# Performance work log

Measured on AMD Instinct MI355X. Metric: run time of the kernel, lower is better.

The kernel has to match this reference:

```python
import jax, jax.numpy as jnp
import numpy as np

B, T, C, H = 4, 1024, 1024, 16
D = C // H  # head dim = 64
EPS = 1e-5


def _layernorm(x, g, b):
    m = jnp.mean(x, axis=-1, keepdims=True)
    v = jnp.var(x, axis=-1, keepdims=True)
    return (x - m) / jnp.sqrt(v + EPS) * g + b


def setup_inputs() -> dict:
    key = jax.random.key(0)
    ks = jax.random.split(key, 8)
    s = 0.02  # GPT-style init scale
    w = lambda k, shp: (jax.random.normal(k, shp, jnp.float32) * s)
    return {
        "x": jax.random.normal(ks[0], (B, T, C), jnp.float32),
        "ln1_g": jnp.ones((C,), jnp.float32), "ln1_b": jnp.zeros((C,), jnp.float32),
        "wq": w(ks[1], (C, C)), "bq": jnp.zeros((C,), jnp.float32),
        "wk": w(ks[2], (C, C)), "bk": jnp.zeros((C,), jnp.float32),
        "wv": w(ks[3], (C, C)), "bv": jnp.zeros((C,), jnp.float32),
        "wo": w(ks[4], (C, C)), "bo": jnp.zeros((C,), jnp.float32),
        "ln2_g": jnp.ones((C,), jnp.float32), "ln2_b": jnp.zeros((C,), jnp.float32),
        "w1": w(ks[5], (C, 4 * C)), "b1": jnp.zeros((4 * C,), jnp.float32),
        "w2": w(ks[6], (4 * C, C)), "b2": jnp.zeros((C,), jnp.float32),
    }


def reference(x, ln1_g, ln1_b, wq, bq, wk, bk, wv, bv, wo, bo,
              ln2_g, ln2_b, w1, b1, w2, b2):
    # --- causal self-attention branch: x = x + attn(ln1(x)) ---
    h = _layernorm(x, ln1_g, ln1_b)
    q = (h @ wq + bq).reshape(B, T, H, D)
    k = (h @ wk + bk).reshape(B, T, H, D)
    v = (h @ wv + bv).reshape(B, T, H, D)
    att = jnp.einsum('bqhd,bkhd->bhqk', q, k) * (1.0 / np.sqrt(D).astype(np.float32))
    causal = jnp.tril(jnp.ones((T, T), bool))
    att = jnp.where(causal, att, -jnp.inf)
    att = jax.nn.softmax(att, axis=-1)  # dropout p=0 -> identity
    y = jnp.einsum('bhqk,bkhd->bqhd', att, v).reshape(B, T, C)
    x = x + (y @ wo + bo)
    # --- MLP branch: x = x + mlp(ln2(x)) ---
    h2 = _layernorm(x, ln2_g, ln2_b)
    m = jax.nn.gelu(h2 @ w1 + b1, approximate=False)  # torch nn.GELU default = exact erf
    x = x + (m @ w2 + b2)
    return x
```

## Files before the change

### kernel.cpp

```cpp
#include <hip/hip_runtime.h>
#include <hip/hip_bf16.h>
#include <math.h>

#define B_ 4
#define T_ 1024
#define C_ 1024
#define H_ 16
#define D_ 64
#define M_ (B_*T_)

typedef __bf16 bf16;
typedef __bf16 bf16x8 __attribute__((ext_vector_type(8)));
typedef float  f32x4  __attribute__((ext_vector_type(4)));

#define MFMA16(a, b, c) __builtin_amdgcn_mfma_f32_16x16x32_bf16((a), (b), (c), 0, 0, 0)

__device__ __forceinline__ void gload16(const void* g, void* l) {
  __builtin_amdgcn_global_load_lds((const __attribute__((address_space(1))) void*)g,
                                   (__attribute__((address_space(3))) void*)l,
                                   16, 0, 0);
}

__global__ __launch_bounds__(256) void wconvT(const float* __restrict__ W,
                                              bf16* __restrict__ WT, int K, int N) {
  __shared__ float tile[32][33];
  int n0 = blockIdx.x * 32, k0 = blockIdx.y * 32;
  int tx = threadIdx.x & 31, ty = threadIdx.x >> 5;
#pragma unroll
  for (int i = ty; i < 32; i += 8)
    tile[i][tx] = W[(size_t)(k0 + i) * N + n0 + tx];
  __syncthreads();
#pragma unroll
  for (int i = ty; i < 32; i += 8)
    WT[(size_t)(n0 + i) * K + k0 + tx] = (bf16)tile[tx][i];
}

__global__ __launch_bounds__(256) void bcat(const float* __restrict__ a,
                                            const float* __restrict__ b,
                                            const float* __restrict__ c,
                                            float* __restrict__ o) {
  int i = blockIdx.x * 256 + threadIdx.x;
  o[i] = (i < 1024) ? a[i] : ((i < 2048) ? b[i - 1024] : c[i - 2048]);
}

__global__ __launch_bounds__(256) void ln_k(const float* __restrict__ x,
                                            const float* __restrict__ g,
                                            const float* __restrict__ b,
                                            bf16* __restrict__ out) {
  int row = blockIdx.x;
  int t = threadIdx.x;
  float4 xv = ((const float4*)(x + (size_t)row * C_))[t];
  float s  = xv.x + xv.y + xv.z + xv.w;
  float ss = xv.x*xv.x + xv.y*xv.y + xv.z*xv.z + xv.w*xv.w;
#pragma unroll
  for (int m = 32; m; m >>= 1) { s += __shfl_xor(s, m); ss += __shfl_xor(ss, m); }
  __shared__ float red[8];
  int wid = t >> 6;
  if ((t & 63) == 0) { red[wid] = s; red[4 + wid] = ss; }
  __syncthreads();
  s  = red[0] + red[1] + red[2] + red[3];
  ss = red[4] + red[5] + red[6] + red[7];
  float mean = s * (1.0f / C_);
  float var  = ss * (1.0f / C_) - mean * mean;
  float inv  = rsqrtf(var + 1e-5f);
  float4 gv = ((const float4*)g)[t];
  float4 bv = ((const float4*)b)[t];
  bf16* o = out + (size_t)row * C_ + t * 4;
  o[0] = (bf16)((xv.x - mean) * inv * gv.x + bv.x);
  o[1] = (bf16)((xv.y - mean) * inv * gv.y + bv.y);
  o[2] = (bf16)((xv.z - mean) * inv * gv.z + bv.z);
  o[3] = (bf16)((xv.w - mean) * inv * gv.w + bv.w);
}

template <int BM, int BN, int WM, int WN, int EPI>
__global__ __launch_bounds__(WM*WN*64, 4)
void gemms(const bf16* __restrict__ A, const bf16* __restrict__ BT,
           const float* __restrict__ bias, const float* __restrict__ res,
           void* __restrict__ outp, int N, int K, int gx) {
  constexpr int NT = WM * WN * 64;
  constexpr int FM = BM / WM / 16, FN = BN / WN / 16;
  constexpr int RA = BM / 32, RB = BN / 32;
  __shared__ __align__(16) bf16 smem[(BM + BN) * 64];
  bf16* sA = smem;
  bf16* sB = smem + BM * 64;
  const int tid = threadIdx.x, lane = tid & 63, wid = tid >> 6;
  const int wr = wid / WN, wc = wid % WN;

  int bid = blockIdx.x;
  const int nwg = gridDim.x;
  if (!(nwg & 7)) bid = (bid & 7) * (nwg >> 3) + (bid >> 3);
  const int bx = bid % gx, by = bid / gx;
  const size_t am0 = (size_t)bx * BM, bn0 = (size_t)by * BN;

  f32x4 acc[FM][FN];
  const f32x4 fz = {0.f, 0.f, 0.f, 0.f};
#pragma unroll
  for (int m = 0; m < FM; ++m)
#pragma unroll
    for (int n = 0; n < FN; ++n) acc[m][n] = fz;

  const int srow = tid >> 3;
  const int sg = (tid & 7) ^ (srow & 7);
  const bf16* ag = A  + (am0 + srow) * (size_t)K + sg * 8;
  const bf16* bg = BT + (bn0 + srow) * (size_t)K + sg * 8;

  const int arow = lane & 15;
  const int g0 = (((lane >> 4))     ^ (lane & 7)) * 8;
  const int g1 = (((lane >> 4) + 4) ^ (lane & 7)) * 8;
  const int nt = K >> 6;

#pragma unroll
  for (int r = 0; r < RA; ++r)
    gload16(ag + (size_t)(r * 32) * K, sA + r * 2048 + tid * 8);
#pragma unroll
  for (int r = 0; r < RB; ++r)
    gload16(bg + (size_t)(r * 32) * K, sB + r * 2048 + tid * 8);

  for (int t = 0; t < nt; ++t) {
    __syncthreads();

    const bf16* pa = sA + (wr * (BM / WM) + arow) * 64;
    const bf16* pb = sB + (wc * (BN / WN) + arow) * 64;
    bf16x8 a[FM], b[FN];
#pragma unroll
    for (int m = 0; m < FM; ++m) a[m] = *(const bf16x8*)(pa + m * 16 * 64 + g0);
#pragma unroll
    for (int n = 0; n < FN; ++n) b[n] = *(const bf16x8*)(pb + n * 16 * 64 + g0);
#pragma unroll
    for (int m = 0; m < FM; ++m)
#pragma unroll
      for (int n = 0; n < FN; ++n)
        acc[m][n] = MFMA16(a[m], b[n], acc[m][n]);
    bf16x8 a1[FM], b1[FN];
#pragma unroll
    for (int m = 0; m < FM; ++m) a1[m] = *(const bf16x8*)(pa + m * 16 * 64 + g1);
#pragma unroll
    for (int n = 0; n < FN; ++n) b1[n] = *(const bf16x8*)(pb + n * 16 * 64 + g1);

    __syncthreads();

    if (t + 1 < nt) {
#pragma unroll
      for (int r = 0; r < RA; ++r)
        gload16(ag + (size_t)(t + 1) * 64 + (size_t)(r * 32) * K,
                sA + r * 2048 + tid * 8);
#pragma unroll
      for (int r = 0; r < RB; ++r)
        gload16(bg + (size_t)(t + 1) * 64 + (size_t)(r * 32) * K,
                sB + r * 2048 + tid * 8);
    }
#pragma unroll
    for (int m = 0; m < FM; ++m)
#pragma unroll
      for (int n = 0; n < FN; ++n)
        acc[m][n] = MFMA16(a1[m], b1[n], acc[m][n]);
  }

  if constexpr (EPI != 2) {
#pragma unroll
    for (int m = 0; m < FM; ++m) {
      const int row0 = wr * (BM / WM) + m * 16 + (lane >> 4) * 4;
#pragma unroll
      for (int n = 0; n < FN; ++n) {
        const int col = wc * (BN / WN) + n * 16 + (lane & 15);
        const float bv = bias[bn0 + col];
#pragma unroll
        for (int j = 0; j < 4; ++j) {
          float v = acc[m][n][j] + bv;
          if constexpr (EPI == 1) v = 0.5f * v * (1.0f + erff(v * 0.70710678118f));
          const int rr = row0 + j;
          smem[rr * BN + (((col >> 3) ^ (rr & 7)) << 3) + (col & 7)] = (bf16)v;
        }
      }
    }
    __syncthreads();
    constexpr int GR = BN / 8;
    constexpr int SI = BM * BN / (NT * 8);
#pragma unroll
    for (int i = 0; i < SI; ++i) {
      const int idx = i * NT + tid;
      const int row = idx / GR, g = idx % GR;
      *(bf16x8*)((bf16*)outp + (am0 + row) * N + bn0 + g * 8) =
          *(const bf16x8*)(smem + row * BN + ((g ^ (row & 7)) << 3));
    }
  } else {
    constexpr int PR = BM / WM;
    float* sf = (float*)smem;
#pragma unroll
    for (int h = 0; h < WM; ++h) {
      __syncthreads();
      if (wr == h) {
#pragma unroll
        for (int m = 0; m < FM; ++m) {
          const int lr0 = m * 16 + (lane >> 4) * 4;
#pragma unroll
          for (int n = 0; n < FN; ++n) {
            const int col = wc * (BN / WN) + n * 16 + (lane & 15);
            const float bv = bias[bn0 + col];
#pragma unroll
            for (int j = 0; j < 4; ++j)
              sf[(lr0 + j) * BN + col] = acc[m][n][j] + bv;
          }
        }
      }
      __syncthreads();
      constexpr int SI = PR * BN / (NT * 4);
#pragma unroll
      for (int i = 0; i < SI; ++i) {
        const int flat = (i * NT + tid) * 4;
        const int row = flat / BN, c = flat % BN;
        const size_t gi = (am0 + h * PR + row) * N + bn0 + c;
        float4 rv = *(const float4*)(res + gi);
        float4 sv = *(const float4*)(sf + row * BN + c);
        rv.x += sv.x; rv.y += sv.y; rv.z += sv.z; rv.w += sv.w;
        *(float4*)((float*)outp + gi) = rv;
      }
    }
  }
}

__global__ __launch_bounds__(256) void attn_k(const bf16* __restrict__ Q,
                                              const bf16* __restrict__ Kb,
                                              const bf16* __restrict__ Vb,
                                              bf16* __restrict__ Y, int ld) {
  int bh = blockIdx.x;
  int b = bh >> 4, h = bh & 15;
  int qt = (int)gridDim.y - 1 - (int)blockIdx.y;
  int q0 = qt * 64;
  int tid = threadIdx.x, wid = tid >> 6, lane = tid & 63;

  __shared__ __align__(16) bf16 sK[64 * 64];
  __shared__ __align__(16) bf16 sVT[64 * 64];
  __shared__ __align__(16) bf16 sP[4][16 * 64];

  const size_t rowQ = (size_t)(b * T_ + q0 + wid * 16 + (lane & 15)) * ld + h * 64 + (lane >> 4) * 8;
  bf16x8 qf0 = *(const bf16x8*)(Q + rowQ);
  bf16x8 qf1 = *(const bf16x8*)(Q + rowQ + 32);

  float m_run[4] = {-1e30f, -1e30f, -1e30f, -1e30f};
  float l_run[4] = {0.f, 0.f, 0.f, 0.f};
  const f32x4 fz = {0.f, 0.f, 0.f, 0.f};
  f32x4 o[4];
#pragma unroll
  for (int i = 0; i < 4; ++i) o[i] = fz;

  const int kgr = (lane & 7) ^ (lane >> 3);
  const bf16* kg = Kb + (size_t)(b * T_ + wid * 16 + (lane >> 3)) * ld + h * 64 + kgr * 8;
  bf16* lk = sK + (wid * 16) * 64;

  const int g0 = (((lane >> 4))     ^ (lane & 7)) * 8;
  const int g1 = (((lane >> 4) + 4) ^ (lane & 7)) * 8;

  for (int kt = 0; kt <= qt; ++kt) {
    int k0 = kt * 64;
#pragma unroll
    for (int i = 0; i < 2; ++i)
      gload16(kg + ((size_t)(k0 + i * 8)) * ld, lk + i * 8 * 64);
#pragma unroll
    for (int c = 0; c < 2; ++c) {
      const int r = lane, sl = wid + 4 * c;
      bf16x8 vv = *(const bf16x8*)(Vb + (size_t)(b * T_ + k0 + r) * ld + h * 64 + sl * 8);
#pragma unroll
      for (int j = 0; j < 8; ++j)
        sVT[(sl * 8 + j) * 64 + ((((r >> 3) ^ j) << 3) | (r & 7))] = vv[j];
    }
    __syncthreads();

    f32x4 s[4];
#pragma unroll
    for (int ni = 0; ni < 4; ++ni) {
      const bf16* kr = sK + (ni * 16 + (lane & 15)) * 64;
      bf16x8 kf0 = *(const bf16x8*)(kr + g0);
      bf16x8 kf1 = *(const bf16x8*)(kr + g1);
      f32x4 t = fz;
      t = MFMA16(qf0, kf0, t);
      t = MFMA16(qf1, kf1, t);
      s[ni] = t;
    }

    int rbase = q0 + wid * 16 + (lane >> 4) * 4;
    int cbase = k0 + (lane & 15);
    float tm[4] = {-1e30f, -1e30f, -1e30f, -1e30f};
#pragma unroll
    for (int ni = 0; ni < 4; ++ni)
#pragma unroll
      for (int j = 0; j < 4; ++j) {
        float v = s[ni][j] * 0.125f;
        if (cbase + ni * 16 > rbase + j) v = -1e30f;
        s[ni][j] = v;
        tm[j] = fmaxf(tm[j], v);
      }
#pragma unroll
    for (int j = 0; j < 4; ++j)
#pragma unroll
      for (int mk = 1; mk < 16; mk <<= 1)
        tm[j] = fmaxf(tm[j], __shfl_xor(tm[j], mk));

    float fac[4], rs[4] = {0.f, 0.f, 0.f, 0.f};
#pragma unroll
    for (int j = 0; j < 4; ++j) {
      float mn = fmaxf(m_run[j], tm[j]);
      fac[j] = __expf(m_run[j] - mn);
      m_run[j] = mn;
    }
#pragma unroll
    for (int ni = 0; ni < 4; ++ni)
#pragma unroll
      for (int j = 0; j < 4; ++j) {
        float p = __expf(s[ni][j] - m_run[j]);
        rs[j] += p;
        const int crow = (lane >> 4) * 4 + j;
        const int cg = (ni * 2 + ((lane & 15) >> 3)) ^ (crow & 7);
        sP[wid][crow * 64 + (cg << 3) + (lane & 7)] = (bf16)p;
      }
#pragma unroll
    for (int j = 0; j < 4; ++j) {
#pragma unroll
      for (int mk = 1; mk < 16; mk <<= 1)
        rs[j] += __shfl_xor(rs[j], mk);
      l_run[j] = l_run[j] * fac[j] + rs[j];
    }
#pragma unroll
    for (int df = 0; df < 4; ++df)
#pragma unroll
      for (int j = 0; j < 4; ++j)
        o[df][j] *= fac[j];

#pragma unroll
    for (int kk = 0; kk < 2; ++kk) {
      const int gk = kk ? g1 : g0;
      bf16x8 pf = *(const bf16x8*)(sP[wid] + (lane & 15) * 64 + gk);
#pragma unroll
      for (int df = 0; df < 4; ++df) {
        bf16x8 vf = *(const bf16x8*)(sVT + (df * 16 + (lane & 15)) * 64 + gk);
        o[df] = MFMA16(pf, vf, o[df]);
      }
    }
    __syncthreads();
  }

#pragma unroll
  for (int df = 0; df < 4; ++df)
#pragma unroll
    for (int j = 0; j < 4; ++j) {
      int row = q0 + wid * 16 + (lane >> 4) * 4 + j;
      int d = df * 16 + (lane & 15);
      Y[(size_t)(b * T_ + row) * C_ + h * 64 + d] = (bf16)(o[df][j] / l_run[j]);
    }
}

extern "C" void kernel_launch(void* const* d_in, const int* in_sizes, int n_in,
                              void* d_out, int out_size, void* d_ws, size_t ws_size,
                              hipStream_t stream) {
  (void)in_sizes; (void)n_in; (void)out_size; (void)ws_size;
  const float* x    = (const float*)d_in[0];
  const float* ln1g = (const float*)d_in[1];
  const float* ln1b = (const float*)d_in[2];
  const float* wq   = (const float*)d_in[3];
  const float* bq   = (const float*)d_in[4];
  const float* wk   = (const float*)d_in[5];
  const float* bk   = (const float*)d_in[6];
  const float* wv   = (const float*)d_in[7];
  const float* bv   = (const float*)d_in[8];
  const float* wo   = (const float*)d_in[9];
  const float* bo   = (const float*)d_in[10];
  const float* ln2g = (const float*)d_in[11];
  const float* ln2b = (const float*)d_in[12];
  const float* w1   = (const float*)d_in[13];
  const float* b1   = (const float*)d_in[14];
  const float* w2   = (const float*)d_in[15];
  const float* b2   = (const float*)d_in[16];

  char* ws = (char*)d_ws;
  const size_t MB = 1024 * 1024;
  bf16* WqkvT = (bf16*)(ws +  0 * MB);
  bf16* WoT   = (bf16*)(ws +  6 * MB);
  bf16* W1T   = (bf16*)(ws +  8 * MB);
  bf16* W2T   = (bf16*)(ws + 16 * MB);
  bf16* hbuf  = (bf16*)(ws + 24 * MB);
  bf16* qkv   = (bf16*)(ws + 32 * MB);
  bf16* yb    = (bf16*)(ws + 56 * MB);
  bf16* mb    = (bf16*)(ws + 32 * MB);
  float* x1   = (float*)(ws + 64 * MB);
  float* bqkv = (float*)d_out;

  dim3 blk(256);
  wconvT<<<dim3(32, 32),  blk, 0, stream>>>(wq, WqkvT,                 1024, 1024);
  wconvT<<<dim3(32, 32),  blk, 0, stream>>>(wk, WqkvT + 1024 * 1024,   1024, 1024);
  wconvT<<<dim3(32, 32),  blk, 0, stream>>>(wv, WqkvT + 2048 * 1024,   1024, 1024);
  wconvT<<<dim3(32, 32),  blk, 0, stream>>>(wo, WoT, 1024, 1024);
  wconvT<<<dim3(128, 32), blk, 0, stream>>>(w1, W1T, 1024, 4096);
  wconvT<<<dim3(32, 128), blk, 0, stream>>>(w2, W2T, 4096, 1024);
  bcat<<<12, blk, 0, stream>>>(bq, bk, bv, bqkv);

  ln_k<<<M_, blk, 0, stream>>>(x, ln1g, ln1b, hbuf);
  gemms<128,128,2,2,0><<<768,  blk, 0, stream>>>(hbuf, WqkvT, bqkv, nullptr, qkv, 3072, 1024, 32);
  attn_k<<<dim3(64, 16), blk, 0, stream>>>(qkv, qkv + 1024, qkv + 2048, yb, 3072);
  gemms<64,128,2,2,2><<<512,   blk, 0, stream>>>(yb, WoT, bo, x, x1, 1024, 1024, 64);
  ln_k<<<M_, blk, 0, stream>>>(x1, ln2g, ln2b, hbuf);
  gemms<128,128,2,2,1><<<1024, blk, 0, stream>>>(hbuf, W1T, b1, nullptr, mb, 4096, 1024, 32);
  gemms<64,128,2,2,2><<<512,   blk, 0, stream>>>(mb, W2T, b2, x1, (float*)d_out, 1024, 4096, 64);
}
```

Measured before the change: 232.7 us.

## Double-buffer K/V tiles in attention and merge weight conversions into one launch

```diff
diff --git a/kernel.cpp b/kernel.cpp
--- a/kernel.cpp
+++ b/kernel.cpp
@@ -21,11 +21,30 @@
                                    16, 0, 0);
 }
 
-__global__ __launch_bounds__(256) void wconvT(const float* __restrict__ W,
-                                              bf16* __restrict__ WT, int K, int N) {
+__global__ __launch_bounds__(256) void wprep(const float* __restrict__ wq,
+                                             const float* __restrict__ wk,
+                                             const float* __restrict__ wv,
+                                             const float* __restrict__ wo,
+                                             const float* __restrict__ w1,
+                                             const float* __restrict__ w2,
+                                             bf16* __restrict__ WqkvT,
+                                             bf16* __restrict__ WoT,
+                                             bf16* __restrict__ W1T,
+                                             bf16* __restrict__ W2T) {
   __shared__ float tile[32][33];
-  int n0 = blockIdx.x * 32, k0 = blockIdx.y * 32;
-  int tx = threadIdx.x & 31, ty = threadIdx.x >> 5;
+  const int b = blockIdx.x;
+  const float* W; bf16* WT; int K, N, n0, k0;
+  if (b < 3072)      { const int w = b >> 10, t = b & 1023;
+                       W = (w == 0) ? wq : ((w == 1) ? wk : wv);
+                       WT = WqkvT + (size_t)w * 1024 * 1024;
+                       K = 1024; N = 1024; n0 = (t & 31) * 32; k0 = (t >> 5) * 32; }
+  else if (b < 4096) { const int t = b - 3072; W = wo; WT = WoT;
+                       K = 1024; N = 1024; n0 = (t & 31) * 32; k0 = (t >> 5) * 32; }
+  else if (b < 8192) { const int t = b - 4096; W = w1; WT = W1T;
+                       K = 1024; N = 4096; n0 = (t & 127) * 32; k0 = (t >> 7) * 32; }
+  else               { const int t = b - 8192; W = w2; WT = W2T;
+                       K = 4096; N = 1024; n0 = (t & 31) * 32; k0 = (t >> 5) * 32; }
+  const int tx = threadIdx.x & 31, ty = threadIdx.x >> 5;
 #pragma unroll
   for (int i = ty; i < 32; i += 8)
     tile[i][tx] = W[(size_t)(k0 + i) * N + n0 + tx];
@@ -229,8 +248,8 @@
   int q0 = qt * 64;
   int tid = threadIdx.x, wid = tid >> 6, lane = tid & 63;
 
-  __shared__ __align__(16) bf16 sK[64 * 64];
-  __shared__ __align__(16) bf16 sVT[64 * 64];
+  __shared__ __align__(16) bf16 sK[2][64 * 64];
+  __shared__ __align__(16) bf16 sVT[2][64 * 64];
   __shared__ __align__(16) bf16 sP[4][16 * 64];
 
   const size_t rowQ = (size_t)(b * T_ + q0 + wid * 16 + (lane & 15)) * ld + h * 64 + (lane >> 4) * 8;
@@ -246,30 +265,44 @@
 
   const int kgr = (lane & 7) ^ (lane >> 3);
   const bf16* kg = Kb + (size_t)(b * T_ + wid * 16 + (lane >> 3)) * ld + h * 64 + kgr * 8;
-  bf16* lk = sK + (wid * 16) * 64;
+  const int lkoff = (wid * 16) * 64;
+  const bf16* vg = Vb + (size_t)(b * T_ + lane) * ld + h * 64;
 
   const int g0 = (((lane >> 4))     ^ (lane & 7)) * 8;
   const int g1 = (((lane >> 4) + 4) ^ (lane & 7)) * 8;
 
+  gload16(kg,                   sK[0] + lkoff);
+  gload16(kg + (size_t)8 * ld,  sK[0] + lkoff + 8 * 64);
+  {
+    bf16x8 v0 = *(const bf16x8*)(vg + wid * 8);
+    bf16x8 v1 = *(const bf16x8*)(vg + (wid + 4) * 8);
+#pragma unroll
+    for (int j = 0; j < 8; ++j) {
+      const int pc = ((((lane >> 3) ^ j) << 3) | (lane & 7));
+      sVT[0][(wid * 8 + j) * 64 + pc]       = v0[j];
+      sVT[0][((wid + 4) * 8 + j) * 64 + pc] = v1[j];
+    }
+  }
+
   for (int kt = 0; kt <= qt; ++kt) {
-    int k0 = kt * 64;
-#pragma unroll
-    for (int i = 0; i < 2; ++i)
-      gload16(kg + ((size_t)(k0 + i * 8)) * ld, lk + i * 8 * 64);
-#pragma unroll
-    for (int c = 0; c < 2; ++c) {
-      const int r = lane, sl = wid + 4 * c;
-      bf16x8 vv = *(const bf16x8*)(Vb + (size_t)(b * T_ + k0 + r) * ld + h * 64 + sl * 8);
-#pragma unroll
-      for (int j = 0; j < 8; ++j)
-        sVT[(sl * 8 + j) * 64 + ((((r >> 3) ^ j) << 3) | (r & 7))] = vv[j];
-    }
+    const int cur = kt & 1, nxt = cur ^ 1;
+    const bool pf = (kt < qt);
     __syncthreads();
 
+    bf16x8 vn0, vn1;
+    if (pf) {
+      const size_t k1 = (size_t)(kt + 1) * 64;
+      gload16(kg + k1 * ld,        sK[nxt] + lkoff);
+      gload16(kg + (k1 + 8) * ld,  sK[nxt] + lkoff + 8 * 64);
+      vn0 = *(const bf16x8*)(vg + k1 * ld + wid * 8);
+      vn1 = *(const bf16x8*)(vg + k1 * ld + (wid + 4) * 8);
+    }
+
+    const int k0 = kt * 64;
     f32x4 s[4];
 #pragma unroll
     for (int ni = 0; ni < 4; ++ni) {
-      const bf16* kr = sK + (ni * 16 + (lane & 15)) * 64;
+      const bf16* kr = sK[cur] + (ni * 16 + (lane & 15)) * 64;
       bf16x8 kf0 = *(const bf16x8*)(kr + g0);
       bf16x8 kf1 = *(const bf16x8*)(kr + g1);
       f32x4 t = fz;
@@ -329,14 +362,22 @@
 #pragma unroll
     for (int kk = 0; kk < 2; ++kk) {
       const int gk = kk ? g1 : g0;
-      bf16x8 pf = *(const bf16x8*)(sP[wid] + (lane & 15) * 64 + gk);
+      bf16x8 pf8 = *(const bf16x8*)(sP[wid] + (lane & 15) * 64 + gk);
 #pragma unroll
       for (int df = 0; df < 4; ++df) {
-        bf16x8 vf = *(const bf16x8*)(sVT + (df * 16 + (lane & 15)) * 64 + gk);
-        o[df] = MFMA16(pf, vf, o[df]);
-      }
-    }
-    __syncthreads();
+        bf16x8 vf = *(const bf16x8*)(sVT[cur] + (df * 16 + (lane & 15)) * 64 + gk);
+        o[df] = MFMA16(pf8, vf, o[df]);
+      }
+    }
+
+    if (pf) {
+#pragma unroll
+      for (int j = 0; j < 8; ++j) {
+        const int pc = ((((lane >> 3) ^ j) << 3) | (lane & 7));
+        sVT[nxt][(wid * 8 + j) * 64 + pc]       = vn0[j];
+        sVT[nxt][((wid + 4) * 8 + j) * 64 + pc] = vn1[j];
+      }
+    }
   }
 
 #pragma unroll
@@ -385,12 +426,7 @@
   float* bqkv = (float*)d_out;
 
   dim3 blk(256);
-  wconvT<<<dim3(32, 32),  blk, 0, stream>>>(wq, WqkvT,                 1024, 1024);
-  wconvT<<<dim3(32, 32),  blk, 0, stream>>>(wk, WqkvT + 1024 * 1024,   1024, 1024);
-  wconvT<<<dim3(32, 32),  blk, 0, stream>>>(wv, WqkvT + 2048 * 1024,   1024, 1024);
-  wconvT<<<dim3(32, 32),  blk, 0, stream>>>(wo, WoT, 1024, 1024);
-  wconvT<<<dim3(128, 32), blk, 0, stream>>>(w1, W1T, 1024, 4096);
-  wconvT<<<dim3(32, 128), blk, 0, stream>>>(w2, W2T, 4096, 1024);
+  wprep<<<12288, blk, 0, stream>>>(wq, wk, wv, wo, w1, w2, WqkvT, WoT, W1T, W2T);
   bcat<<<12, blk, 0, stream>>>(bq, bk, bv, bqkv);
 
   ln_k<<<M_, blk, 0, stream>>>(x, ln1g, ln1b, hbuf);
```

New measurement: 218.2 us. -6.2%, faster.
